# Kernel optimization log

Measured on AMD Instinct MI355X. Metric: run time of the kernel, lower is better.

Reference implementation:

```python
import jax, jax.numpy as jnp
import numpy as np

SEQ, BATCH, V = 200, 4096, 50000


def setup_inputs() -> dict:
    key = jax.random.key(0)
    k_text, k_w, k_b = jax.random.split(key, 3)
    text = jax.random.randint(k_text, (SEQ, BATCH), 0, V, dtype=jnp.int64 if jax.config.jax_enable_x64 else jnp.int32)
    w_weight = jax.random.normal(k_w, (1, V), dtype=jnp.float32) * 0.05
    w_bias = jax.random.normal(k_b, (1,), dtype=jnp.float32) * 0.05
    return {"text": text, "w_weight": w_weight, "w_bias": w_bias}


def reference(text, w_weight, w_bias):
    # text: [seq, batch] int token ids; w_weight: [1, V]; w_bias: [1]
    seq, batch = text.shape
    vocab = w_weight.shape[1]
    # Counter over unique tokens per document with +=1 per unique value
    # => binary PRESENCE matrix [batch, V] (duplicates collapse to 1).
    presence = jnp.zeros((batch, vocab), dtype=jnp.float32)
    presence = presence.at[jnp.arange(batch)[None, :], text].set(1.0)
    # Linear(V, 1): [batch, V] @ [V, 1] + bias -> [batch, 1]
    return presence @ w_weight.T + w_bias
```

## Files before the change

### kernel.cpp

```cpp
#include <hip/hip_runtime.h>


#define SEQ    200
#define BATCH  4096
#define COLS   8
#define TSLOTS 512
#define NTOK   (SEQ * COLS)

__global__ __launch_bounds__(256) void MNB_24111946400019_kernel(
    const int* __restrict__ text,
    const float* __restrict__ w,
    const float* __restrict__ bias,
    float* __restrict__ out)
{
    __shared__ int staged[NTOK];
    __shared__ int table[COLS * TSLOTS];

    const int t  = threadIdx.x;
    const int c0 = blockIdx.x * COLS;

    {
        const int4 m1 = make_int4(-1, -1, -1, -1);
        int4* tb = (int4*)table;
        #pragma unroll
        for (int i = 0; i < 4; ++i) tb[t + 256 * i] = m1;
    }

    for (int idx = t; idx < NTOK; idx += 256) {
        const int s = idx >> 3;
        const int j = idx & (COLS - 1);
        staged[idx] = text[s * BATCH + c0 + j];
    }
    __syncthreads();

    for (int idx = t; idx < NTOK; idx += 256) {
        const int tok = staged[idx];
        const int j   = idx & (COLS - 1);
        unsigned h = ((unsigned)tok * 2654435761u) >> 23;
        int* tb = &table[j * TSLOTS];
        for (;;) {
            const int prev = atomicCAS(&tb[h], -1, tok);
            if (prev == -1 || prev == tok) break;
            h = (h + 1) & (TSLOTS - 1);
        }
    }
    __syncthreads();

    const int j = t >> 5;
    const int l = t & 31;
    float sum = 0.0f;
    #pragma unroll
    for (int k = 0; k < TSLOTS / 32; ++k) {
        const int tok = table[j * TSLOTS + l + 32 * k];
        if (tok >= 0) sum += w[tok];
    }

    #pragma unroll
    for (int off = 16; off > 0; off >>= 1)
        sum += __shfl_xor(sum, off, 64);

    if (l == 0) out[c0 + j] = sum + bias[0];
}

extern "C" void kernel_launch(void* const* d_in, const int* in_sizes, int n_in,
                              void* d_out, int out_size, void* d_ws, size_t ws_size,
                              hipStream_t stream) {
    const int*   text = (const int*)d_in[0];
    const float* w    = (const float*)d_in[1];
    const float* bias = (const float*)d_in[2];
    float* out = (float*)d_out;

    MNB_24111946400019_kernel<<<BATCH / COLS, 256, 0, stream>>>(text, w, bias, out);
}
```

Measured before the change: 65.87 us.

## Replace per-column hash table with shared-memory bitmap dedup and fused gather

```diff
diff --git a/kernel.cpp b/kernel.cpp
--- a/kernel.cpp
+++ b/kernel.cpp
@@ -3,9 +3,9 @@
 
 #define SEQ    200
 #define BATCH  4096
-#define COLS   8
-#define TSLOTS 512
-#define NTOK   (SEQ * COLS)
+#define VOCAB  50000
+#define COLS   4
+#define WPC    1568
 
 __global__ __launch_bounds__(256) void MNB_24111946400019_kernel(
     const int* __restrict__ text,
@@ -13,53 +13,55 @@
     const float* __restrict__ bias,
     float* __restrict__ out)
 {
-    __shared__ int staged[NTOK];
-    __shared__ int table[COLS * TSLOTS];
+    __shared__ __align__(16) unsigned bm[COLS * WPC];
+    __shared__ float partials[4][COLS];
 
     const int t  = threadIdx.x;
     const int c0 = blockIdx.x * COLS;
+    const int j  = t & (COLS - 1);
 
     {
-        const int4 m1 = make_int4(-1, -1, -1, -1);
-        int4* tb = (int4*)table;
-        #pragma unroll
-        for (int i = 0; i < 4; ++i) tb[t + 256 * i] = m1;
-    }
-
-    for (int idx = t; idx < NTOK; idx += 256) {
-        const int s = idx >> 3;
-        const int j = idx & (COLS - 1);
-        staged[idx] = text[s * BATCH + c0 + j];
+        int4* p = (int4*)bm;
+        const int4 z = make_int4(0, 0, 0, 0);
+        for (int i = t; i < COLS * WPC / 4; i += 256) p[i] = z;
     }
     __syncthreads();
 
-    for (int idx = t; idx < NTOK; idx += 256) {
-        const int tok = staged[idx];
-        const int j   = idx & (COLS - 1);
-        unsigned h = ((unsigned)tok * 2654435761u) >> 23;
-        int* tb = &table[j * TSLOTS];
-        for (;;) {
-            const int prev = atomicCAS(&tb[h], -1, tok);
-            if (prev == -1 || prev == tok) break;
-            h = (h + 1) & (TSLOTS - 1);
-        }
-    }
-    __syncthreads();
+    const int s0 = t >> 2;
+    const int* tp = text + s0 * BATCH + c0 + j;
+    const int tokA = tp[0];
+    const int tokB = tp[64 * BATCH];
+    const int tokC = tp[128 * BATCH];
+    const int tokD = (t < 32) ? tp[192 * BATCH] : 0;
 
-    const int j = t >> 5;
-    const int l = t & 31;
+    unsigned* tb = bm + j * WPC;
     float sum = 0.0f;
-    #pragma unroll
-    for (int k = 0; k < TSLOTS / 32; ++k) {
-        const int tok = table[j * TSLOTS + l + 32 * k];
-        if (tok >= 0) sum += w[tok];
+
+    const unsigned bitA = 1u << (tokA & 31);
+    const unsigned bitB = 1u << (tokB & 31);
+    const unsigned bitC = 1u << (tokC & 31);
+    const unsigned oldA = atomicOr(&tb[tokA >> 5], bitA);
+    const unsigned oldB = atomicOr(&tb[tokB >> 5], bitB);
+    const unsigned oldC = atomicOr(&tb[tokC >> 5], bitC);
+    if (!(oldA & bitA)) sum += w[tokA];
+    if (!(oldB & bitB)) sum += w[tokB];
+    if (!(oldC & bitC)) sum += w[tokC];
+    if (t < 32) {
+        const unsigned bitD = 1u << (tokD & 31);
+        const unsigned oldD = atomicOr(&tb[tokD >> 5], bitD);
+        if (!(oldD & bitD)) sum += w[tokD];
     }
 
     #pragma unroll
-    for (int off = 16; off > 0; off >>= 1)
+    for (int off = 4; off <= 32; off <<= 1)
         sum += __shfl_xor(sum, off, 64);
 
-    if (l == 0) out[c0 + j] = sum + bias[0];
+    if ((t & 63) < COLS) partials[t >> 6][j] = sum;
+    __syncthreads();
+
+    if (t < COLS)
+        out[c0 + t] = partials[0][t] + partials[1][t] + partials[2][t]
+                    + partials[3][t] + bias[0];
 }
 
 extern "C" void kernel_launch(void* const* d_in, const int* in_sizes, int n_in,
```

After: 64.58 us. About the same (-2.0%).
